# Kernel optimization log

Measured on AMD Instinct MI355X. Metric: run time of the kernel, lower is better.

## Reference

```python
import jax, jax.numpy as jnp
import numpy as np

EPS = 1e-5

def _layernorm(x, w, b):
    mu = jnp.mean(x, axis=-1, keepdims=True)
    var = jnp.var(x, axis=-1, keepdims=True)
    return (x - mu) * jax.lax.rsqrt(var + EPS) * w + b

def setup_inputs() -> dict:
    key = jax.random.key(0)
    ks = jax.random.split(key, 8)
    N, C = 768, 128
    s = 1.0 / np.sqrt(C)
    return {
        "pair": jax.random.normal(ks[0], (N, N, C), dtype=jnp.float32),
        "ln_in_w": jnp.ones((C,), jnp.float32),
        "ln_in_b": jnp.zeros((C,), jnp.float32),
        "w_proj": jax.random.uniform(ks[1], (2 * C, C), jnp.float32, -s, s),
        "w_gate": jax.random.uniform(ks[2], (2 * C, C), jnp.float32, -s, s),
        "ln_c_w": jnp.ones((C,), jnp.float32),
        "ln_c_b": jnp.zeros((C,), jnp.float32),
        "w_out": jax.random.uniform(ks[3], (C, C), jnp.float32, -s, s),
        "w_glin": jax.random.uniform(ks[4], (C, C), jnp.float32, -s, s),
    }

def reference(pair, ln_in_w, ln_in_b, w_proj, w_gate, ln_c_w, ln_c_b, w_out, w_glin):
    # pair: [N, N, C]
    x = _layernorm(pair, ln_in_w, ln_in_b)          # input LayerNorm
    proj = x @ w_proj.T                              # [N, N, 2C]
    gate = x @ w_gate.T                              # [N, N, 2C]
    pg = proj * jax.nn.sigmoid(gate)                 # gated projection
    # torch reshape([2C,N,N] -> [C,2,N,N]) interleaves channels:
    a = pg[..., 0::2]                                # [N, N, C]
    b = pg[..., 1::2]                                # [N, N, C]
    # outgoing: out[i,j,c] = sum_k a[i,k,c] * b[j,k,c]
    out = jnp.einsum('ikc,jkc->ijc', a, b)           # [N, N, C]
    out = _layernorm(out, ln_c_w, ln_c_b)
    out = out @ w_out.T
    out = out * jax.nn.sigmoid(x @ w_glin.T)         # output gate
    return out
```

## Files before the change

kernel.cpp:

```cpp
#include <hip/hip_runtime.h>
#include <stdint.h>


#define NN_F (768 * 768)

typedef float f32x4 __attribute__((ext_vector_type(4)));
typedef __bf16 bf16x8 __attribute__((ext_vector_type(8)));

#define AS1 __attribute__((address_space(1)))
#define AS3 __attribute__((address_space(3)))

__device__ __forceinline__ unsigned short f2b(float f) {
  unsigned u = __builtin_bit_cast(unsigned, f);
  u = u + 0x7fffu + ((u >> 16) & 1u);
  return (unsigned short)(u >> 16);
}
__device__ __forceinline__ float b2f(unsigned short s) {
  return __builtin_bit_cast(float, ((unsigned)s) << 16);
}
__device__ __forceinline__ float sigf(float x) {
  return 1.0f / (1.0f + __expf(-x));
}

__global__ __launch_bounds__(256) void k0_weights(
    const float* __restrict__ w_proj, const float* __restrict__ w_gate,
    const float* __restrict__ w_glin, const float* __restrict__ w_out,
    unsigned short* __restrict__ Wcat) {
  int idx = blockIdx.x * 256 + threadIdx.x;
  int r = idx >> 7, k = idx & 127;
  float v;
  if (r < 512) {
    int c = r >> 2, tt = r & 3;
    int row = 2 * c + (tt >> 1);
    v = (tt & 1) ? w_gate[row * 128 + k] : w_proj[row * 128 + k];
  } else if (r < 640) {
    v = w_glin[(r - 512) * 128 + k];
  } else {
    v = w_out[(r - 640) * 128 + k];
  }
  Wcat[idx] = f2b(v);
}

__global__ __launch_bounds__(256) void k1_proj(
    const float* __restrict__ pair, const float* __restrict__ lnw,
    const float* __restrict__ lnb, const unsigned short* __restrict__ Wcat,
    unsigned short* __restrict__ a_t, unsigned short* __restrict__ b_t,
    unsigned short* __restrict__ g) {
  __shared__ float xs[64 * 132];
  __shared__ float red[8][64];
  __shared__ float muA[64], rsA[64];
  __shared__ unsigned short wbuf[32 * 512];

  const int t = threadIdx.x;
  const int l = t & 63, w = t >> 6;
  const int lm = l & 15, lq = l >> 4;
  const size_t p0 = (size_t)blockIdx.x * 64;

  const float* src = pair + p0 * 128;
#pragma unroll
  for (int v = 0; v < 8; ++v) {
    int fi = (v * 256 + t) * 4;
    int p = fi >> 7, c = fi & 127;
    f32x4 d = *(const f32x4*)(src + fi);
    *(f32x4*)&xs[p * 132 + c] = d;
  }
  __syncthreads();
  {
    int p = t & 63, q = t >> 6;
    float s1 = 0.f, s2 = 0.f;
#pragma unroll
    for (int cc = 0; cc < 32; ++cc) {
      float x = xs[p * 132 + q * 32 + cc];
      s1 += x;
      s2 += x * x;
    }
    red[q][p] = s1;
    red[q + 4][p] = s2;
  }
  __syncthreads();
  if (t < 64) {
    float s1 = red[0][t] + red[1][t] + red[2][t] + red[3][t];
    float s2 = red[4][t] + red[5][t] + red[6][t] + red[7][t];
    float mu = s1 * (1.f / 128.f);
    float var = s2 * (1.f / 128.f) - mu * mu;
    muA[t] = mu;
    rsA[t] = rsqrtf(var + 1e-5f);
  }
  __syncthreads();
  bf16x8 xfr[4][4];
#pragma unroll
  for (int pt = 0; pt < 4; ++pt) {
    int p = pt * 16 + lm;
    float mu = muA[p], rs = rsA[p];
#pragma unroll
    for (int kt = 0; kt < 4; ++kt) {
      int ks = kt * 32 + lq * 8;
      union { bf16x8 v; unsigned short u[8]; } fr;
#pragma unroll
      for (int j = 0; j < 8; ++j) {
        float x = xs[p * 132 + ks + j];
        fr.u[j] = f2b((x - mu) * rs * lnw[ks + j] + lnb[ks + j]);
      }
      xfr[pt][kt] = fr.v;
    }
  }
  for (int wc = 0; wc < 5; ++wc) {
    __syncthreads();
    int r0 = wc * 128;
#pragma unroll
    for (int at2 = 0; at2 < 2; ++at2) {
      int at = w * 2 + at2;
#pragma unroll
      for (int kt = 0; kt < 4; ++kt) {
        const unsigned short* gp =
            Wcat + (size_t)(r0 + at * 16 + lm) * 128 + kt * 32 + lq * 8;
        __builtin_amdgcn_global_load_lds((const AS1 void*)gp,
                                         (AS3 void*)(wbuf + (at * 4 + kt) * 512),
                                         16, 0, 0);
      }
    }
    __builtin_amdgcn_s_waitcnt(0x0f70);
    f32x4 acc[2][4];
#pragma unroll
    for (int a2 = 0; a2 < 2; ++a2)
#pragma unroll
      for (int pt = 0; pt < 4; ++pt) acc[a2][pt] = (f32x4){0.f, 0.f, 0.f, 0.f};
#pragma unroll
    for (int at2 = 0; at2 < 2; ++at2) {
      int at = w * 2 + at2;
      bf16x8 af[4];
#pragma unroll
      for (int kt = 0; kt < 4; ++kt)
        af[kt] = *(const bf16x8*)&wbuf[(at * 4 + kt) * 512 + l * 8];
#pragma unroll
      for (int pt = 0; pt < 4; ++pt)
#pragma unroll
        for (int kt = 0; kt < 4; ++kt)
          acc[at2][pt] = __builtin_amdgcn_mfma_f32_16x16x32_bf16(
              af[kt], xfr[pt][kt], acc[at2][pt], 0, 0, 0);
    }
#pragma unroll
    for (int at2 = 0; at2 < 2; ++at2) {
      int rbase = r0 + (w * 2 + at2) * 16 + lq * 4;
#pragma unroll
      for (int pt = 0; pt < 4; ++pt) {
        f32x4 d = acc[at2][pt];
        size_t point = p0 + pt * 16 + lm;
        if (wc < 4) {
          int c = rbase >> 2;
          a_t[(size_t)c * NN_F + point] = f2b(d[0] * sigf(d[1]));
          b_t[(size_t)c * NN_F + point] = f2b(d[2] * sigf(d[3]));
        } else {
          int co = rbase - 512;
          union { unsigned long long ll; unsigned short u[4]; } pk;
          pk.u[0] = f2b(sigf(d[0]));
          pk.u[1] = f2b(sigf(d[1]));
          pk.u[2] = f2b(sigf(d[2]));
          pk.u[3] = f2b(sigf(d[3]));
          *(unsigned long long*)&g[point * 128 + co] = pk.ll;
        }
      }
    }
  }
}

__global__ __launch_bounds__(256) void k2_einsum(
    const unsigned short* __restrict__ a_t, const unsigned short* __restrict__ b_t,
    unsigned short* __restrict__ o_t) {
  __shared__ unsigned short As[128 * 32];
  __shared__ unsigned short Bs[128 * 32];
  const int t = threadIdx.x;
  const int l = t & 63, w = t >> 6;
  const int lm = l & 15, lq = l >> 4;
  const int c = blockIdx.z;
  const int m0 = blockIdx.y * 128, n0 = blockIdx.x * 128;
  const unsigned short* Ac = a_t + (size_t)c * NN_F;
  const unsigned short* Bc = b_t + (size_t)c * NN_F;
  const int wi = w >> 1, wj = w & 1;
  const int lrow = l >> 2, lk = (l & 3) * 8;
  f32x4 acc[4][4];
#pragma unroll
  for (int ti = 0; ti < 4; ++ti)
#pragma unroll
    for (int tj = 0; tj < 4; ++tj) acc[ti][tj] = (f32x4){0.f, 0.f, 0.f, 0.f};

  for (int kb = 0; kb < 24; ++kb) {
    __syncthreads();
#pragma unroll
    for (int h = 0; h < 2; ++h) {
      int row = w * 32 + h * 16 + lrow;
      __builtin_amdgcn_global_load_lds(
          (const AS1 void*)(Ac + (size_t)(m0 + row) * 768 + kb * 32 + lk),
          (AS3 void*)(As + (w * 32 + h * 16) * 32), 16, 0, 0);
      __builtin_amdgcn_global_load_lds(
          (const AS1 void*)(Bc + (size_t)(n0 + row) * 768 + kb * 32 + lk),
          (AS3 void*)(Bs + (w * 32 + h * 16) * 32), 16, 0, 0);
    }
    __builtin_amdgcn_s_waitcnt(0x0f70);
    __syncthreads();
    bf16x8 af[4], bfr[4];
#pragma unroll
    for (int ti = 0; ti < 4; ++ti)
      af[ti] = *(const bf16x8*)&As[(wi * 64 + ti * 16 + lm) * 32 + lq * 8];
#pragma unroll
    for (int tj = 0; tj < 4; ++tj)
      bfr[tj] = *(const bf16x8*)&Bs[(wj * 64 + tj * 16 + lm) * 32 + lq * 8];
#pragma unroll
    for (int ti = 0; ti < 4; ++ti)
#pragma unroll
      for (int tj = 0; tj < 4; ++tj)
        acc[ti][tj] = __builtin_amdgcn_mfma_f32_16x16x32_bf16(
            af[ti], bfr[tj], acc[ti][tj], 0, 0, 0);
  }
  unsigned short* Oc = o_t + (size_t)c * NN_F;
#pragma unroll
  for (int ti = 0; ti < 4; ++ti) {
    int ib = m0 + wi * 64 + ti * 16 + lq * 4;
#pragma unroll
    for (int tj = 0; tj < 4; ++tj) {
      int j = n0 + wj * 64 + tj * 16 + lm;
      f32x4 d = acc[ti][tj];
#pragma unroll
      for (int r = 0; r < 4; ++r) Oc[(size_t)(ib + r) * 768 + j] = f2b(d[r]);
    }
  }
}

__global__ __launch_bounds__(256) void k3_out(
    const unsigned short* __restrict__ o_t, const float* __restrict__ lnw,
    const float* __restrict__ lnb, const unsigned short* __restrict__ Wcat,
    const unsigned short* __restrict__ g, float* __restrict__ out) {
  __shared__ float ys[64 * 132];
  __shared__ float red[8][64];
  __shared__ float muA[64], rsA[64];
  __shared__ unsigned short wbuf[32 * 512];

  const int t = threadIdx.x;
  const int l = t & 63, w = t >> 6;
  const int lm = l & 15, lq = l >> 4;
  const size_t pblk = (size_t)blockIdx.x * 64;
  const int i = (int)(pblk / 768), j0 = (int)(pblk % 768);

#pragma unroll
  for (int at2 = 0; at2 < 2; ++at2) {
    int at = w * 2 + at2;
#pragma unroll
    for (int kt = 0; kt < 4; ++kt) {
      const unsigned short* gp =
          Wcat + (size_t)(640 + at * 16 + lm) * 128 + kt * 32 + lq * 8;
      __builtin_amdgcn_global_load_lds(
          (const AS1 void*)gp, (AS3 void*)(wbuf + (at * 4 + kt) * 512), 16, 0, 0);
    }
  }

  {
    int jj = t & 63, cg = t >> 6;
#pragma unroll
    for (int it = 0; it < 32; ++it) {
      int cc = cg * 32 + it;
      ys[jj * 132 + cc] = b2f(o_t[(size_t)cc * NN_F + (size_t)i * 768 + j0 + jj]);
    }
  }
  __syncthreads();
  {
    int p = t & 63, q = t >> 6;
    float s1 = 0.f, s2 = 0.f;
#pragma unroll
    for (int cc = 0; cc < 32; ++cc) {
      float x = ys[p * 132 + q * 32 + cc];
      s1 += x;
      s2 += x * x;
    }
    red[q][p] = s1;
    red[q + 4][p] = s2;
  }
  __syncthreads();
  if (t < 64) {
    float s1 = red[0][t] + red[1][t] + red[2][t] + red[3][t];
    float s2 = red[4][t] + red[5][t] + red[6][t] + red[7][t];
    float mu = s1 * (1.f / 128.f);
    float var = s2 * (1.f / 128.f) - mu * mu;
    muA[t] = mu;
    rsA[t] = rsqrtf(var + 1e-5f);
  }
  __syncthreads();
  bf16x8 yfr[4][4];
#pragma unroll
  for (int pt = 0; pt < 4; ++pt) {
    int p = pt * 16 + lm;
    float mu = muA[p], rs = rsA[p];
#pragma unroll
    for (int kt = 0; kt < 4; ++kt) {
      int ks = kt * 32 + lq * 8;
      union { bf16x8 v; unsigned short u[8]; } fr;
#pragma unroll
      for (int j = 0; j < 8; ++j) {
        float x = ys[p * 132 + ks + j];
        fr.u[j] = f2b((x - mu) * rs * lnw[ks + j] + lnb[ks + j]);
      }
      yfr[pt][kt] = fr.v;
    }
  }
  __builtin_amdgcn_s_waitcnt(0x0f70);
  f32x4 acc[2][4];
#pragma unroll
  for (int a2 = 0; a2 < 2; ++a2)
#pragma unroll
    for (int pt = 0; pt < 4; ++pt) acc[a2][pt] = (f32x4){0.f, 0.f, 0.f, 0.f};
#pragma unroll
  for (int at2 = 0; at2 < 2; ++at2) {
    int at = w * 2 + at2;
    bf16x8 af[4];
#pragma unroll
    for (int kt = 0; kt < 4; ++kt)
      af[kt] = *(const bf16x8*)&wbuf[(at * 4 + kt) * 512 + l * 8];
#pragma unroll
    for (int pt = 0; pt < 4; ++pt)
#pragma unroll
      for (int kt = 0; kt < 4; ++kt)
        acc[at2][pt] = __builtin_amdgcn_mfma_f32_16x16x32_bf16(
            af[kt], yfr[pt][kt], acc[at2][pt], 0, 0, 0);
  }
#pragma unroll
  for (int at2 = 0; at2 < 2; ++at2) {
    int ob = (w * 2 + at2) * 16 + lq * 4;
#pragma unroll
    for (int pt = 0; pt < 4; ++pt) {
      size_t point = pblk + pt * 16 + lm;
      f32x4 d = acc[at2][pt];
      union { unsigned long long ll; unsigned short u[4]; } pk;
      pk.ll = *(const unsigned long long*)(g + point * 128 + ob);
      f32x4 r;
      r[0] = d[0] * b2f(pk.u[0]);
      r[1] = d[1] * b2f(pk.u[1]);
      r[2] = d[2] * b2f(pk.u[2]);
      r[3] = d[3] * b2f(pk.u[3]);
      *(f32x4*)&out[point * 128 + ob] = r;
    }
  }
}

extern "C" void kernel_launch(void* const* d_in, const int* in_sizes, int n_in,
                              void* d_out, int out_size, void* d_ws, size_t ws_size,
                              hipStream_t stream) {
  const float* pair = (const float*)d_in[0];
  const float* ln_in_w = (const float*)d_in[1];
  const float* ln_in_b = (const float*)d_in[2];
  const float* w_proj = (const float*)d_in[3];
  const float* w_gate = (const float*)d_in[4];
  const float* ln_c_w = (const float*)d_in[5];
  const float* ln_c_b = (const float*)d_in[6];
  const float* w_out = (const float*)d_in[7];
  const float* w_glin = (const float*)d_in[8];
  float* out = (float*)d_out;

  char* ws = (char*)d_ws;
  const size_t SZ = (size_t)150994944;
  unsigned short* a_t = (unsigned short*)(ws);
  unsigned short* b_t = (unsigned short*)(ws + SZ);
  unsigned short* o_t = (unsigned short*)(ws + 2 * SZ);
  unsigned short* g = (unsigned short*)(ws + 3 * SZ);
  unsigned short* Wcat = (unsigned short*)(ws + 4 * SZ);

  hipLaunchKernelGGL(k0_weights, dim3(384), dim3(256), 0, stream,
                     w_proj, w_gate, w_glin, w_out, Wcat);
  hipLaunchKernelGGL(k1_proj, dim3(9216), dim3(256), 0, stream,
                     pair, ln_in_w, ln_in_b, Wcat, a_t, b_t, g);
  hipLaunchKernelGGL(k2_einsum, dim3(6, 6, 128), dim3(256), 0, stream,
                     a_t, b_t, o_t);
  hipLaunchKernelGGL(k3_out, dim3(9216), dim3(256), 0, stream,
                     o_t, ln_c_w, ln_c_b, Wcat, g, out);
}
```

Baseline: 1.148 ms.

## Shrink LDS in projection and output kernels; load weights directly into registers

In k1_proj, the input LayerNorm is now computed in registers with wave shuffles and the normalized rows are stored to LDS as bf16. This replaces the fp32 staging buffer, the shared reduction buffers and two barriers. Both k1 and k3 now load weight fragments straight from global memory into registers instead of copying them through an LDS weight buffer, and both set launch bounds to ask for 4 blocks per CU. k3 also reads o_t two bf16 values at a time and pads its LDS rows to 133 floats to reduce bank conflicts. The aim is higher occupancy and fewer LDS round-trips and syncs, at the cost of repeated global weight reads per block and more register pressure.

```diff
diff --git a/kernel.cpp b/kernel.cpp
--- a/kernel.cpp
+++ b/kernel.cpp
@@ -41,104 +41,76 @@
   Wcat[idx] = f2b(v);
 }
 
-__global__ __launch_bounds__(256) void k1_proj(
+__global__ __launch_bounds__(256, 4) void k1_proj(
     const float* __restrict__ pair, const float* __restrict__ lnw,
     const float* __restrict__ lnb, const unsigned short* __restrict__ Wcat,
     unsigned short* __restrict__ a_t, unsigned short* __restrict__ b_t,
     unsigned short* __restrict__ g) {
-  __shared__ float xs[64 * 132];
-  __shared__ float red[8][64];
-  __shared__ float muA[64], rsA[64];
-  __shared__ unsigned short wbuf[32 * 512];
+  __shared__ unsigned short xs[64 * 136];
 
   const int t = threadIdx.x;
   const int l = t & 63, w = t >> 6;
   const int lm = l & 15, lq = l >> 4;
   const size_t p0 = (size_t)blockIdx.x * 64;
-
-  const float* src = pair + p0 * 128;
+  const int sub = t & 31, pp = t >> 5;
+
+  const float* src = pair + (p0 + pp) * 128 + sub * 4;
+  f32x4 x[8];
+#pragma unroll
+  for (int v = 0; v < 8; ++v) x[v] = *(const f32x4*)(src + v * 8 * 128);
+  const f32x4 gw = *(const f32x4*)(lnw + sub * 4);
+  const f32x4 gb = *(const f32x4*)(lnb + sub * 4);
+
 #pragma unroll
   for (int v = 0; v < 8; ++v) {
-    int fi = (v * 256 + t) * 4;
-    int p = fi >> 7, c = fi & 127;
-    f32x4 d = *(const f32x4*)(src + fi);
-    *(f32x4*)&xs[p * 132 + c] = d;
+    f32x4 xv = x[v];
+    float s1 = (xv[0] + xv[1]) + (xv[2] + xv[3]);
+    float s2 = (xv[0] * xv[0] + xv[1] * xv[1]) + (xv[2] * xv[2] + xv[3] * xv[3]);
+#pragma unroll
+    for (int m = 1; m <= 16; m <<= 1) {
+      s1 += __shfl_xor(s1, m, 64);
+      s2 += __shfl_xor(s2, m, 64);
+    }
+    float mu = s1 * (1.f / 128.f);
+    float rs = rsqrtf(s2 * (1.f / 128.f) - mu * mu + 1e-5f);
+    union { unsigned long long ll; unsigned short us[4]; } pk;
+#pragma unroll
+    for (int e = 0; e < 4; ++e)
+      pk.us[e] = f2b((xv[e] - mu) * rs * gw[e] + gb[e]);
+    *(unsigned long long*)&xs[(pp + 8 * v) * 136 + sub * 4] = pk.ll;
   }
   __syncthreads();
-  {
-    int p = t & 63, q = t >> 6;
-    float s1 = 0.f, s2 = 0.f;
-#pragma unroll
-    for (int cc = 0; cc < 32; ++cc) {
-      float x = xs[p * 132 + q * 32 + cc];
-      s1 += x;
-      s2 += x * x;
-    }
-    red[q][p] = s1;
-    red[q + 4][p] = s2;
-  }
-  __syncthreads();
-  if (t < 64) {
-    float s1 = red[0][t] + red[1][t] + red[2][t] + red[3][t];
-    float s2 = red[4][t] + red[5][t] + red[6][t] + red[7][t];
-    float mu = s1 * (1.f / 128.f);
-    float var = s2 * (1.f / 128.f) - mu * mu;
-    muA[t] = mu;
-    rsA[t] = rsqrtf(var + 1e-5f);
-  }
-  __syncthreads();
-  bf16x8 xfr[4][4];
-#pragma unroll
-  for (int pt = 0; pt < 4; ++pt) {
-    int p = pt * 16 + lm;
-    float mu = muA[p], rs = rsA[p];
-#pragma unroll
-    for (int kt = 0; kt < 4; ++kt) {
-      int ks = kt * 32 + lq * 8;
-      union { bf16x8 v; unsigned short u[8]; } fr;
-#pragma unroll
-      for (int j = 0; j < 8; ++j) {
-        float x = xs[p * 132 + ks + j];
-        fr.u[j] = f2b((x - mu) * rs * lnw[ks + j] + lnb[ks + j]);
-      }
-      xfr[pt][kt] = fr.v;
-    }
-  }
+
   for (int wc = 0; wc < 5; ++wc) {
-    __syncthreads();
-    int r0 = wc * 128;
-#pragma unroll
-    for (int at2 = 0; at2 < 2; ++at2) {
-      int at = w * 2 + at2;
-#pragma unroll
-      for (int kt = 0; kt < 4; ++kt) {
-        const unsigned short* gp =
-            Wcat + (size_t)(r0 + at * 16 + lm) * 128 + kt * 32 + lq * 8;
-        __builtin_amdgcn_global_load_lds((const AS1 void*)gp,
-                                         (AS3 void*)(wbuf + (at * 4 + kt) * 512),
-                                         16, 0, 0);
-      }
-    }
-    __builtin_amdgcn_s_waitcnt(0x0f70);
+    const int r0 = wc * 128;
+    bf16x8 wfr[2][4];
+#pragma unroll
+    for (int at2 = 0; at2 < 2; ++at2)
+#pragma unroll
+      for (int kt = 0; kt < 4; ++kt)
+        wfr[at2][kt] = *(const bf16x8*)&Wcat[
+            (size_t)(r0 + (w * 2 + at2) * 16 + lm) * 128 + kt * 32 + lq * 8];
+
     f32x4 acc[2][4];
 #pragma unroll
     for (int a2 = 0; a2 < 2; ++a2)
 #pragma unroll
       for (int pt = 0; pt < 4; ++pt) acc[a2][pt] = (f32x4){0.f, 0.f, 0.f, 0.f};
-#pragma unroll
-    for (int at2 = 0; at2 < 2; ++at2) {
-      int at = w * 2 + at2;
-      bf16x8 af[4];
+
+#pragma unroll
+    for (int pt = 0; pt < 4; ++pt) {
+      bf16x8 xf[4];
 #pragma unroll
       for (int kt = 0; kt < 4; ++kt)
-        af[kt] = *(const bf16x8*)&wbuf[(at * 4 + kt) * 512 + l * 8];
-#pragma unroll
-      for (int pt = 0; pt < 4; ++pt)
+        xf[kt] = *(const bf16x8*)&xs[(pt * 16 + lm) * 136 + kt * 32 + lq * 8];
+#pragma unroll
+      for (int at2 = 0; at2 < 2; ++at2)
 #pragma unroll
         for (int kt = 0; kt < 4; ++kt)
           acc[at2][pt] = __builtin_amdgcn_mfma_f32_16x16x32_bf16(
-              af[kt], xfr[pt][kt], acc[at2][pt], 0, 0, 0);
-    }
+              wfr[at2][kt], xf[kt], acc[at2][pt], 0, 0, 0);
+    }
+
 #pragma unroll
     for (int at2 = 0; at2 < 2; ++at2) {
       int rbase = r0 + (w * 2 + at2) * 16 + lq * 4;
@@ -226,14 +198,13 @@
   }
 }
 
-__global__ __launch_bounds__(256) void k3_out(
+__global__ __launch_bounds__(256, 4) void k3_out(
     const unsigned short* __restrict__ o_t, const float* __restrict__ lnw,
     const float* __restrict__ lnb, const unsigned short* __restrict__ Wcat,
     const unsigned short* __restrict__ g, float* __restrict__ out) {
-  __shared__ float ys[64 * 132];
+  __shared__ float ys[64 * 133];
   __shared__ float red[8][64];
   __shared__ float muA[64], rsA[64];
-  __shared__ unsigned short wbuf[32 * 512];
 
   const int t = threadIdx.x;
   const int l = t & 63, w = t >> 6;
@@ -241,24 +212,23 @@
   const size_t pblk = (size_t)blockIdx.x * 64;
   const int i = (int)(pblk / 768), j0 = (int)(pblk % 768);
 
-#pragma unroll
-  for (int at2 = 0; at2 < 2; ++at2) {
-    int at = w * 2 + at2;
-#pragma unroll
-    for (int kt = 0; kt < 4; ++kt) {
-      const unsigned short* gp =
-          Wcat + (size_t)(640 + at * 16 + lm) * 128 + kt * 32 + lq * 8;
-      __builtin_amdgcn_global_load_lds(
-          (const AS1 void*)gp, (AS3 void*)(wbuf + (at * 4 + kt) * 512), 16, 0, 0);
-    }
-  }
+  bf16x8 wfr[2][4];
+#pragma unroll
+  for (int at2 = 0; at2 < 2; ++at2)
+#pragma unroll
+    for (int kt = 0; kt < 4; ++kt)
+      wfr[at2][kt] = *(const bf16x8*)&Wcat[
+          (size_t)(640 + (w * 2 + at2) * 16 + lm) * 128 + kt * 32 + lq * 8];
 
   {
-    int jj = t & 63, cg = t >> 6;
-#pragma unroll
-    for (int it = 0; it < 32; ++it) {
-      int cc = cg * 32 + it;
-      ys[jj * 132 + cc] = b2f(o_t[(size_t)cc * NN_F + (size_t)i * 768 + j0 + jj]);
+    int jd = t & 31, ch0 = t >> 5;
+    const unsigned short* base = o_t + (size_t)i * 768 + j0 + jd * 2;
+#pragma unroll
+    for (int v = 0; v < 16; ++v) {
+      int cc = ch0 + 8 * v;
+      unsigned d = *(const unsigned*)(base + (size_t)cc * NN_F);
+      ys[(jd * 2) * 133 + cc] = b2f((unsigned short)(d & 0xffffu));
+      ys[(jd * 2 + 1) * 133 + cc] = b2f((unsigned short)(d >> 16));
     }
   }
   __syncthreads();
@@ -267,9 +237,9 @@
     float s1 = 0.f, s2 = 0.f;
 #pragma unroll
     for (int cc = 0; cc < 32; ++cc) {
-      float x = ys[p * 132 + q * 32 + cc];
-      s1 += x;
-      s2 += x * x;
+      float xv = ys[p * 133 + q * 32 + cc];
+      s1 += xv;
+      s2 += xv * xv;
     }
     red[q][p] = s1;
     red[q + 4][p] = s2;
@@ -295,13 +265,12 @@
       union { bf16x8 v; unsigned short u[8]; } fr;
 #pragma unroll
       for (int j = 0; j < 8; ++j) {
-        float x = ys[p * 132 + ks + j];
-        fr.u[j] = f2b((x - mu) * rs * lnw[ks + j] + lnb[ks + j]);
+        float xv = ys[p * 133 + ks + j];
+        fr.u[j] = f2b((xv - mu) * rs * lnw[ks + j] + lnb[ks + j]);
       }
       yfr[pt][kt] = fr.v;
     }
   }
-  __builtin_amdgcn_s_waitcnt(0x0f70);
   f32x4 acc[2][4];
 #pragma unroll
   for (int a2 = 0; a2 < 2; ++a2)
@@ -309,17 +278,12 @@
     for (int pt = 0; pt < 4; ++pt) acc[a2][pt] = (f32x4){0.f, 0.f, 0.f, 0.f};
 #pragma unroll
   for (int at2 = 0; at2 < 2; ++at2) {
-    int at = w * 2 + at2;
-    bf16x8 af[4];
-#pragma unroll
-    for (int kt = 0; kt < 4; ++kt)
-      af[kt] = *(const bf16x8*)&wbuf[(at * 4 + kt) * 512 + l * 8];
 #pragma unroll
     for (int pt = 0; pt < 4; ++pt)
 #pragma unroll
       for (int kt = 0; kt < 4; ++kt)
         acc[at2][pt] = __builtin_amdgcn_mfma_f32_16x16x32_bf16(
-            af[kt], yfr[pt][kt], acc[at2][pt], 0, 0, 0);
+            wfr[at2][kt], yfr[pt][kt], acc[at2][pt], 0, 0, 0);
   }
 #pragma unroll
   for (int at2 = 0; at2 < 2; ++at2) {
```

Result: slower. 1.243 ms (+8.3%).
